# Performance work log

Hardware: AMD Instinct MI355X
Metric: run time of the kernel (lower is better)

Reference implementation:

```python
import jax, jax.numpy as jnp
import numpy as np

N_NODES = 100000
N_EDGES = 1600000
D_IN, D_HID, D_OUT = 128, 128, 64


def setup_inputs() -> dict:
    key = jax.random.key(0)
    ks = jax.random.split(key, 6)
    x = jax.random.normal(ks[0], (N_NODES, D_IN), dtype=jnp.float32)
    edge_index = jax.random.randint(ks[1], (2, N_EDGES), 0, N_NODES, dtype=jnp.int64)
    s1 = 1.0 / np.sqrt(D_IN)
    s2 = 1.0 / np.sqrt(D_HID)
    return {
        "x": x,
        "edge_index": edge_index,
        "Wl1": jax.random.uniform(ks[2], (D_HID, D_IN), jnp.float32, -s1, s1),
        "bl1": jnp.zeros((D_HID,), jnp.float32),
        "Wr1": jax.random.uniform(ks[3], (D_HID, D_IN), jnp.float32, -s1, s1),
        "Wl2": jax.random.uniform(ks[4], (D_OUT, D_HID), jnp.float32, -s2, s2),
        "bl2": jnp.zeros((D_OUT,), jnp.float32),
        "Wr2": jax.random.uniform(ks[5], (D_OUT, D_HID), jnp.float32, -s2, s2),
    }


def _sage_conv(x, src, dst, Wl, bl, Wr, n_nodes):
    # mean-aggregate neighbor features src -> dst
    agg = jax.ops.segment_sum(x[src], dst, num_segments=n_nodes)  # [N, d_in]
    deg = jax.ops.segment_sum(jnp.ones((src.shape[0],), x.dtype), dst, num_segments=n_nodes)
    agg = agg / jnp.maximum(deg, 1.0)[:, None]
    # PyG SAGEConv: lin_l(agg) + lin_r(x), bias only on lin_l
    return agg @ Wl.T + bl + x @ Wr.T


def reference(x, edge_index, Wl1, bl1, Wr1, Wl2, bl2, Wr2):
    src, dst = edge_index[0], edge_index[1]
    n = x.shape[0]
    h = _sage_conv(x, src, dst, Wl1, bl1, Wr1, n)
    h = jax.nn.relu(h)
    # dropout is identity in eval mode (training=False)
    out = _sage_conv(h, src, dst, Wl2, bl2, Wr2, n)
    return out
```

## Files before the change

kernel.cpp:

```cpp
#include <hip/hip_runtime.h>

#define N_NODES_C 100000
#define N_EDGES_C 1600000
#define NTILES_C 6250
#define CAP_C 48
#define NBUCK_C 196
#define BCAP_C 10240
#define EPB_C 4096

typedef __attribute__((ext_vector_type(8))) short short8;
typedef __attribute__((ext_vector_type(4))) short short4v;
typedef __attribute__((ext_vector_type(4))) float floatx4;

static __device__ __forceinline__ unsigned short f2bf(float f) {
    union { float f; unsigned int u; } c; c.f = f;
    unsigned int u = c.u;
    unsigned int lsb = (u >> 16) & 1u;
    u += 0x7fffu + lsb;
    return (unsigned short)(u >> 16);
}
static __device__ __forceinline__ float bf2f(unsigned short h) {
    union { unsigned int u; float f; } c; c.u = ((unsigned int)h) << 16;
    return c.f;
}

__global__ void bucket_kernel(const int* __restrict__ src, const int* __restrict__ dst,
                              int* __restrict__ gcur, int2* __restrict__ bucket, int E) {
    __shared__ int2 sedge[EPB_C];
    __shared__ int lcnt[NBUCK_C];
    __shared__ int lbase[NBUCK_C];
    __shared__ int lcur[NBUCK_C];
    const int tid = threadIdx.x;
    const int e0 = blockIdx.x * EPB_C;
    const int n = min(EPB_C, E - e0);

    if (tid < NBUCK_C) { lcnt[tid] = 0; lcur[tid] = 0; }
    for (int i = tid; i < n; i += 256) {
        sedge[i] = make_int2(src[e0 + i], dst[e0 + i]);
    }
    __syncthreads();
    for (int i = tid; i < n; i += 256) {
        atomicAdd(&lcnt[sedge[i].y >> 9], 1);
    }
    __syncthreads();
    if (tid < NBUCK_C) {
        int c = lcnt[tid];
        lbase[tid] = (c > 0) ? atomicAdd(&gcur[tid], c) : 0;
    }
    __syncthreads();
    for (int i = tid; i < n; i += 256) {
        int2 e = sedge[i];
        int b = e.y >> 9;
        int p = lbase[b] + atomicAdd(&lcur[b], 1);
        if (p < BCAP_C) bucket[b * BCAP_C + p] = e;
    }
}

__global__ void csr_build_kernel(const int* __restrict__ gcur, const int2* __restrict__ bucket,
                                 int* __restrict__ cnt, int* __restrict__ csr, int N) {
    __shared__ int lcnt[512];
    const int b = blockIdx.x;
    const int tid = threadIdx.x;
    const int d0 = b << 9;
    const int ne = min(gcur[b], BCAP_C);
    lcnt[tid] = 0; lcnt[tid + 256] = 0;
    __syncthreads();
    const int2* be = bucket + b * BCAP_C;
    for (int i = tid; i < ne; i += 256) {
        int2 e = be[i];
        int slot = atomicAdd(&lcnt[e.y - d0], 1);
        if (slot < CAP_C) csr[e.y * CAP_C + slot] = e.x;
    }
    __syncthreads();
    for (int d = tid; d < 512; d += 256) {
        int node = d0 + d;
        if (node < N) cnt[node] = lcnt[d];
    }
}

__global__ void pack1_kernel(const float* __restrict__ Wl, const float* __restrict__ Wr,
                             unsigned short* __restrict__ Bhi, unsigned short* __restrict__ Blo,
                             int total) {
    int t = blockIdx.x * 256 + threadIdx.x;
    if (t >= total) return;
    int j  = t & 7;
    int l  = (t >> 3) & 63;
    int ks = (t >> 9) & 7;
    int ct = t >> 12;
    int k = ks * 32 + ((l >> 4) << 3) + j;
    int o = ct * 16 + (l & 15);
    float v = (k < 128) ? Wl[o * 128 + k] : Wr[o * 128 + (k - 128)];
    unsigned short hi = f2bf(v);
    unsigned short lo = f2bf(v - bf2f(hi));
    Bhi[t] = hi;
    Blo[t] = lo;
}

__global__ void pack2_kernel(const float* __restrict__ Wl, const float* __restrict__ Wr,
                             unsigned short* __restrict__ Bhi, unsigned short* __restrict__ Blo,
                             int total) {
    int t = blockIdx.x * 256 + threadIdx.x;
    if (t >= total) return;
    int j  = t & 7;
    int l  = (t >> 3) & 63;
    int ks = (t >> 9) & 3;
    int ct = t >> 11;
    int k = ks * 32 + ((l >> 4) << 3) + j;
    int o = ct * 16 + (l & 15);
    float v = (o < 64) ? Wl[o * 128 + k] : Wr[(o - 64) * 128 + k];
    unsigned short hi = f2bf(v);
    unsigned short lo = f2bf(v - bf2f(hi));
    Bhi[t] = hi;
    Blo[t] = lo;
}

__global__ void tobf_kernel(const float* __restrict__ x, unsigned short* __restrict__ xb,
                            int total8) {
    int t = blockIdx.x * 256 + threadIdx.x;
    if (t >= total8) return;
    const float4* p = (const float4*)x;
    float4 a = p[(size_t)t * 2];
    float4 b = p[(size_t)t * 2 + 1];
    unsigned short r[8] = {f2bf(a.x), f2bf(a.y), f2bf(a.z), f2bf(a.w),
                           f2bf(b.x), f2bf(b.y), f2bf(b.z), f2bf(b.w)};
    *(uint4*)(xb + (size_t)t * 8) = *(uint4*)r;
}

static __device__ __forceinline__ void acc_add8(float* a, uint4 v) {
    unsigned int u[4] = {v.x, v.y, v.z, v.w};
#pragma unroll
    for (int i = 0; i < 4; i++) {
        union { unsigned int x; float f; } lo, hi;
        lo.x = u[i] << 16;
        hi.x = u[i] & 0xffff0000u;
        a[2 * i]     += lo.f;
        a[2 * i + 1] += hi.f;
    }
}

__global__ void agg_bf_kernel(const unsigned short* __restrict__ featb,
                              const int* __restrict__ cnt,
                              const int* __restrict__ csr,
                              unsigned short* __restrict__ aggb, int N) {
    int wid = (blockIdx.x * 256 + threadIdx.x) >> 6;
    if (wid >= N) return;
    int lane = threadIdx.x & 63;
    int q = lane >> 4;
    int c = lane & 15;
    int degc = cnt[wid];
    int deg = min(degc, CAP_C);
    const int* row = csr + wid * CAP_C;
    float acc0[8] = {0.f, 0.f, 0.f, 0.f, 0.f, 0.f, 0.f, 0.f};
    float acc1[8] = {0.f, 0.f, 0.f, 0.f, 0.f, 0.f, 0.f, 0.f};
    int e = q;
    for (; e + 4 < deg; e += 8) {
        int s0 = row[e];
        int s1 = row[e + 4];
        uint4 v0 = *(const uint4*)(featb + (size_t)s0 * 128 + c * 8);
        uint4 v1 = *(const uint4*)(featb + (size_t)s1 * 128 + c * 8);
        acc_add8(acc0, v0);
        acc_add8(acc1, v1);
    }
    if (e < deg) {
        int s0 = row[e];
        uint4 v0 = *(const uint4*)(featb + (size_t)s0 * 128 + c * 8);
        acc_add8(acc0, v0);
    }
    float acc[8];
#pragma unroll
    for (int j = 0; j < 8; j++) {
        float v = acc0[j] + acc1[j];
        v += __shfl_xor(v, 16, 64);
        v += __shfl_xor(v, 32, 64);
        acc[j] = v;
    }
    if (lane < 16) {
        float sc = 1.0f / fmaxf((float)degc, 1.0f);
        unsigned short r[8];
#pragma unroll
        for (int j = 0; j < 8; j++) r[j] = f2bf(acc[j] * sc);
        *(uint4*)(aggb + (size_t)wid * 128 + c * 8) = *(uint4*)r;
    }
}

__launch_bounds__(256, 2)
__global__ void gemm1_kernel(const unsigned short* __restrict__ aggb,
                             const float* __restrict__ xf,
                             const unsigned short* __restrict__ Bhi,
                             const unsigned short* __restrict__ Blo,
                             const float* __restrict__ bias,
                             unsigned short* __restrict__ hbf) {
    constexpr int CTW = 2, NACC = 2;
    __shared__ unsigned short sAhi[16][264];
    __shared__ unsigned short sAlo[16][136];

    const int wave = threadIdx.x >> 6;
    const int lane = threadIdx.x & 63;
    const int quad = lane >> 4;
    const int l16 = lane & 15;

    short8 bhi[CTW][8], blo[CTW][8];
    float bias_v[CTW];
#pragma unroll
    for (int i = 0; i < CTW; i++) {
        int ct = wave * CTW + i;
        bias_v[i] = bias[ct * 16 + l16];
#pragma unroll
        for (int ks = 0; ks < 8; ks++) {
            int off = ((ct * 8 + ks) * 64 + lane) * 8;
            bhi[i][ks] = *(const short8*)(Bhi + off);
            blo[i][ks] = *(const short8*)(Blo + off);
        }
    }

    const int tn = threadIdx.x >> 4;
    const int tc = threadIdx.x & 15;

    for (int tile = blockIdx.x; tile < NTILES_C; tile += gridDim.x) {
        const int node0 = tile * 16;
        const size_t rowa = (size_t)(node0 + tn) * 128;
        *(short8*)&sAhi[tn][tc * 8] = *(const short8*)(aggb + rowa + tc * 8);
#pragma unroll
        for (int r = 0; r < 2; r++) {
            int c2 = tc + r * 16;
            float4 v = *(const float4*)(xf + rowa + c2 * 4);
            short4v hi, lo;
            unsigned short h0 = f2bf(v.x); hi.x = (short)h0; lo.x = (short)f2bf(v.x - bf2f(h0));
            unsigned short h1 = f2bf(v.y); hi.y = (short)h1; lo.y = (short)f2bf(v.y - bf2f(h1));
            unsigned short h2 = f2bf(v.z); hi.z = (short)h2; lo.z = (short)f2bf(v.z - bf2f(h2));
            unsigned short h3 = f2bf(v.w); hi.w = (short)h3; lo.w = (short)f2bf(v.w - bf2f(h3));
            *(short4v*)&sAhi[tn][128 + c2 * 4] = hi;
            *(short4v*)&sAlo[tn][c2 * 4]       = lo;
        }
        __syncthreads();

        floatx4 acc[CTW][NACC];
#pragma unroll
        for (int i = 0; i < CTW; i++)
#pragma unroll
            for (int p = 0; p < NACC; p++)
                acc[i][p] = (floatx4){0.f, 0.f, 0.f, 0.f};

#pragma unroll
        for (int ks = 0; ks < 8; ks++) {
            short8 ahi = *(const short8*)&sAhi[l16][ks * 32 + quad * 8];
            int p = ks & 1;
            if (ks < 4) {
#pragma unroll
                for (int i = 0; i < CTW; i++) {
                    acc[i][p] = __builtin_amdgcn_mfma_f32_16x16x32_bf16(ahi, bhi[i][ks], acc[i][p], 0, 0, 0);
                    acc[i][p] = __builtin_amdgcn_mfma_f32_16x16x32_bf16(ahi, blo[i][ks], acc[i][p], 0, 0, 0);
                }
            } else {
                short8 alo = *(const short8*)&sAlo[l16][(ks - 4) * 32 + quad * 8];
#pragma unroll
                for (int i = 0; i < CTW; i++) {
                    acc[i][p] = __builtin_amdgcn_mfma_f32_16x16x32_bf16(ahi, bhi[i][ks], acc[i][p], 0, 0, 0);
                    acc[i][p] = __builtin_amdgcn_mfma_f32_16x16x32_bf16(alo, bhi[i][ks], acc[i][p], 0, 0, 0);
                    acc[i][p] = __builtin_amdgcn_mfma_f32_16x16x32_bf16(ahi, blo[i][ks], acc[i][p], 0, 0, 0);
                }
            }
        }

#pragma unroll
        for (int i = 0; i < CTW; i++) {
            floatx4 s = acc[i][0];
            s.x += acc[i][1].x; s.y += acc[i][1].y;
            s.z += acc[i][1].z; s.w += acc[i][1].w;
            int o = (wave * CTW + i) * 16 + l16;
            float vals[4] = {s.x, s.y, s.z, s.w};
#pragma unroll
            for (int r = 0; r < 4; r++) {
                int node = node0 + quad * 4 + r;
                float v = fmaxf(vals[r] + bias_v[i], 0.f);
                hbf[(size_t)node * 128 + o] = f2bf(v);
            }
        }
        __syncthreads();
    }
}

__launch_bounds__(256, 2)
__global__ void gemm2_kernel(const unsigned short* __restrict__ hbf,
                             const unsigned short* __restrict__ Bhi,
                             const unsigned short* __restrict__ Blo,
                             const float* __restrict__ bias,
                             unsigned short* __restrict__ g,
                             unsigned short* __restrict__ s2b) {
    constexpr int CTW = 2, NACC = 2;
    __shared__ unsigned short sA[16][136];

    const int wave = threadIdx.x >> 6;
    const int lane = threadIdx.x & 63;
    const int quad = lane >> 4;
    const int l16 = lane & 15;

    short8 bhi[CTW][4], blo[CTW][4];
    float bias_v[CTW];
#pragma unroll
    for (int i = 0; i < CTW; i++) {
        int ct = wave * CTW + i;
        int o = ct * 16 + l16;
        bias_v[i] = (o >= 64) ? bias[o - 64] : 0.f;
#pragma unroll
        for (int ks = 0; ks < 4; ks++) {
            int off = ((ct * 4 + ks) * 64 + lane) * 8;
            bhi[i][ks] = *(const short8*)(Bhi + off);
            blo[i][ks] = *(const short8*)(Blo + off);
        }
    }

    const int tn = threadIdx.x >> 4;
    const int tc = threadIdx.x & 15;

    for (int tile = blockIdx.x; tile < NTILES_C; tile += gridDim.x) {
        const int node0 = tile * 16;
        *(short8*)&sA[tn][tc * 8] = *(const short8*)(hbf + (size_t)(node0 + tn) * 128 + tc * 8);
        __syncthreads();

        floatx4 acc[CTW][NACC];
#pragma unroll
        for (int i = 0; i < CTW; i++)
#pragma unroll
            for (int p = 0; p < NACC; p++)
                acc[i][p] = (floatx4){0.f, 0.f, 0.f, 0.f};

#pragma unroll
        for (int ks = 0; ks < 4; ks++) {
            short8 ahi = *(const short8*)&sA[l16][ks * 32 + quad * 8];
            int p = ks & 1;
#pragma unroll
            for (int i = 0; i < CTW; i++) {
                acc[i][p] = __builtin_amdgcn_mfma_f32_16x16x32_bf16(ahi, bhi[i][ks], acc[i][p], 0, 0, 0);
                acc[i][p] = __builtin_amdgcn_mfma_f32_16x16x32_bf16(ahi, blo[i][ks], acc[i][p], 0, 0, 0);
            }
        }

#pragma unroll
        for (int i = 0; i < CTW; i++) {
            floatx4 s = acc[i][0];
            s.x += acc[i][1].x; s.y += acc[i][1].y;
            s.z += acc[i][1].z; s.w += acc[i][1].w;
            int o = (wave * CTW + i) * 16 + l16;
            float vals[4] = {s.x, s.y, s.z, s.w};
#pragma unroll
            for (int r = 0; r < 4; r++) {
                int node = node0 + quad * 4 + r;
                float v = vals[r] + bias_v[i];
                if (o < 64) g[(size_t)node * 64 + o] = f2bf(v);
                else        s2b[(size_t)node * 64 + (o - 64)] = f2bf(v);
            }
        }
        __syncthreads();
    }
}

static __device__ __forceinline__ void acc_add4(float* a, uint2 v) {
    unsigned int u[2] = {v.x, v.y};
#pragma unroll
    for (int i = 0; i < 2; i++) {
        union { unsigned int x; float f; } lo, hi;
        lo.x = u[i] << 16;
        hi.x = u[i] & 0xffff0000u;
        a[2 * i]     += lo.f;
        a[2 * i + 1] += hi.f;
    }
}

__global__ void agg2e_kernel(const unsigned short* __restrict__ g,
                             const unsigned short* __restrict__ s2b,
                             const int* __restrict__ cnt,
                             const int* __restrict__ csr,
                             float* __restrict__ out, int N) {
    int wid = (blockIdx.x * 256 + threadIdx.x) >> 6;
    if (wid >= N) return;
    int lane = threadIdx.x & 63;
    int q = lane >> 4;
    int c = lane & 15;
    int degc = cnt[wid];
    int deg = min(degc, CAP_C);
    const int* row = csr + wid * CAP_C;
    float acc0[4] = {0.f, 0.f, 0.f, 0.f};
    float acc1[4] = {0.f, 0.f, 0.f, 0.f};
    int e = q;
    for (; e + 4 < deg; e += 8) {
        int s0 = row[e];
        int s1 = row[e + 4];
        uint2 v0 = *(const uint2*)(g + (size_t)s0 * 64 + c * 4);
        uint2 v1 = *(const uint2*)(g + (size_t)s1 * 64 + c * 4);
        acc_add4(acc0, v0);
        acc_add4(acc1, v1);
    }
    if (e < deg) {
        int s0 = row[e];
        uint2 v0 = *(const uint2*)(g + (size_t)s0 * 64 + c * 4);
        acc_add4(acc0, v0);
    }
    float acc[4];
#pragma unroll
    for (int j = 0; j < 4; j++) {
        float v = acc0[j] + acc1[j];
        v += __shfl_xor(v, 16, 64);
        v += __shfl_xor(v, 32, 64);
        acc[j] = v;
    }
    if (lane < 16) {
        float sc = 1.0f / fmaxf((float)degc, 1.0f);
        uint2 sv = *(const uint2*)(s2b + (size_t)wid * 64 + c * 4);
        float s[4];
        {
            union { unsigned int x; float f; } t0, t1, t2, t3;
            t0.x = sv.x << 16; t1.x = sv.x & 0xffff0000u;
            t2.x = sv.y << 16; t3.x = sv.y & 0xffff0000u;
            s[0] = t0.f; s[1] = t1.f; s[2] = t2.f; s[3] = t3.f;
        }
        float4 r;
        r.x = acc[0] * sc + s[0];
        r.y = acc[1] * sc + s[1];
        r.z = acc[2] * sc + s[2];
        r.w = acc[3] * sc + s[3];
        *(float4*)(out + (size_t)wid * 64 + c * 4) = r;
    }
}

extern "C" void kernel_launch(void* const* d_in, const int* in_sizes, int n_in,
                              void* d_out, int out_size, void* d_ws, size_t ws_size,
                              hipStream_t stream) {
    const float* x    = (const float*)d_in[0];
    const int*   ei   = (const int*)d_in[1];
    const float* Wl1  = (const float*)d_in[2];
    const float* bl1  = (const float*)d_in[3];
    const float* Wr1  = (const float*)d_in[4];
    const float* Wl2  = (const float*)d_in[5];
    const float* bl2  = (const float*)d_in[6];
    const float* Wr2  = (const float*)d_in[7];
    float* out = (float*)d_out;

    const int N = N_NODES_C;
    const int E = N_EDGES_C;
    const int* src = ei;
    const int* dst = ei + E;

    char* ws = (char*)d_ws;
    unsigned short* B1hi = (unsigned short*)(ws + 0);
    unsigned short* B1lo = (unsigned short*)(ws + 65536);
    unsigned short* B2hi = (unsigned short*)(ws + 131072);
    unsigned short* B2lo = (unsigned short*)(ws + 163840);
    int*   cnt  = (int*)  (ws + 196608);
    int*   gcur = (int*)  (ws + 598016);
    int*   csr  = (int*)  (ws + 1048576);
    unsigned short* xbf  = (unsigned short*)(ws + 20248576);
    unsigned short* aggb = (unsigned short*)(ws + 45848576);
    unsigned short* hbf  = (unsigned short*)(ws + 71448576);
    unsigned short* g    = aggb;
    unsigned short* s2b  = aggb + 6400000;
    int2*  bucket = (int2*)hbf;

    hipMemsetAsync(gcur, 0, NBUCK_C * sizeof(int), stream);
    bucket_kernel<<<(E + EPB_C - 1) / EPB_C, 256, 0, stream>>>(src, dst, gcur, bucket, E);
    csr_build_kernel<<<NBUCK_C, 256, 0, stream>>>(gcur, bucket, cnt, csr, N);

    pack1_kernel<<<128, 256, 0, stream>>>(Wl1, Wr1, B1hi, B1lo, 128 * 256);
    pack2_kernel<<<64, 256, 0, stream>>>(Wl2, Wr2, B2hi, B2lo, 128 * 128);
    tobf_kernel<<<(N * 16 + 255) / 256, 256, 0, stream>>>(x, xbf, N * 16);

    agg_bf_kernel<<<(N + 3) / 4, 256, 0, stream>>>(xbf, cnt, csr, aggb, N);
    gemm1_kernel<<<512, 256, 0, stream>>>(aggb, x, B1hi, B1lo, bl1, hbf);

    gemm2_kernel<<<512, 256, 0, stream>>>(hbf, B2hi, B2lo, bl2, g, s2b);
    agg2e_kernel<<<(N + 3) / 4, 256, 0, stream>>>(g, s2b, cnt, csr, out, N);
}
```

Measured before the change: 293.5 us.

## Build compact CSR with prefix offsets, fuse prep kernels, widen GEMM tiles

Replaces the fixed-capacity padded neighbor lists (48 slots per node) with a compact CSR. Buckets now hold 256 nodes each, and every edge is packed into a single int. A per-bucket prefix scan produces node offsets, which are stored in a nodeinfo array. The two weight-packing kernels and the fp32-to-bf16 conversion of x are merged into one launch. The aggregation loops are unrolled to four independent accumulators, and both GEMM kernels process 32-node tiles instead of 16. The aim is to cut CSR memory traffic, the cost of the padded layout, and launch overhead, and to expose more memory-level parallelism. The trade-offs are a serial prefix sum over bucket counts done by thread 0 in every block, and more shared memory in csr_build.

```diff
diff --git a/kernel.cpp b/kernel.cpp
--- a/kernel.cpp
+++ b/kernel.cpp
@@ -2,10 +2,9 @@
 
 #define N_NODES_C 100000
 #define N_EDGES_C 1600000
-#define NTILES_C 6250
-#define CAP_C 48
-#define NBUCK_C 196
-#define BCAP_C 10240
+#define NT32_C 3125
+#define NBUCK_C 392
+#define BCAP_C 4800
 #define EPB_C 4096
 
 typedef __attribute__((ext_vector_type(8))) short short8;
@@ -25,8 +24,9 @@
 }
 
 __global__ void bucket_kernel(const int* __restrict__ src, const int* __restrict__ dst,
-                              int* __restrict__ gcur, int2* __restrict__ bucket, int E) {
-    __shared__ int2 sedge[EPB_C];
+                              int* __restrict__ gcur, int* __restrict__ bucket, int E) {
+    __shared__ int ssrc[EPB_C];
+    __shared__ int sdst[EPB_C];
     __shared__ int lcnt[NBUCK_C];
     __shared__ int lbase[NBUCK_C];
     __shared__ int lcur[NBUCK_C];
@@ -34,96 +34,123 @@
     const int e0 = blockIdx.x * EPB_C;
     const int n = min(EPB_C, E - e0);
 
-    if (tid < NBUCK_C) { lcnt[tid] = 0; lcur[tid] = 0; }
+    for (int i = tid; i < NBUCK_C; i += 256) { lcnt[i] = 0; lcur[i] = 0; }
     for (int i = tid; i < n; i += 256) {
-        sedge[i] = make_int2(src[e0 + i], dst[e0 + i]);
+        ssrc[i] = src[e0 + i];
+        sdst[i] = dst[e0 + i];
     }
     __syncthreads();
     for (int i = tid; i < n; i += 256) {
-        atomicAdd(&lcnt[sedge[i].y >> 9], 1);
-    }
-    __syncthreads();
-    if (tid < NBUCK_C) {
-        int c = lcnt[tid];
-        lbase[tid] = (c > 0) ? atomicAdd(&gcur[tid], c) : 0;
+        atomicAdd(&lcnt[sdst[i] >> 8], 1);
+    }
+    __syncthreads();
+    for (int i = tid; i < NBUCK_C; i += 256) {
+        int c = lcnt[i];
+        lbase[i] = (c > 0) ? atomicAdd(&gcur[i], c) : 0;
     }
     __syncthreads();
     for (int i = tid; i < n; i += 256) {
-        int2 e = sedge[i];
-        int b = e.y >> 9;
+        int d = sdst[i];
+        int b = d >> 8;
         int p = lbase[b] + atomicAdd(&lcur[b], 1);
-        if (p < BCAP_C) bucket[b * BCAP_C + p] = e;
-    }
-}
-
-__global__ void csr_build_kernel(const int* __restrict__ gcur, const int2* __restrict__ bucket,
-                                 int* __restrict__ cnt, int* __restrict__ csr, int N) {
-    __shared__ int lcnt[512];
+        if (p < BCAP_C) bucket[b * BCAP_C + p] = (ssrc[i] << 8) | (d & 255);
+    }
+}
+
+__global__ void csr_build_kernel(const int* __restrict__ gcur, const int* __restrict__ bucket,
+                                 int2* __restrict__ nodeinfo, int* __restrict__ csr, int N) {
+    __shared__ int sg[NBUCK_C];
+    __shared__ int lcnt[256];
+    __shared__ int lcur[256];
+    __shared__ int sc[2][256];
+    __shared__ int eord[BCAP_C];
+    __shared__ int sbase_s;
     const int b = blockIdx.x;
     const int tid = threadIdx.x;
-    const int d0 = b << 9;
     const int ne = min(gcur[b], BCAP_C);
-    lcnt[tid] = 0; lcnt[tid + 256] = 0;
-    __syncthreads();
-    const int2* be = bucket + b * BCAP_C;
+
+    for (int i = tid; i < NBUCK_C; i += 256) sg[i] = min(gcur[i], BCAP_C);
+    lcnt[tid] = 0;
+    lcur[tid] = 0;
+    __syncthreads();
+    if (tid == 0) {
+        int s = 0;
+        for (int i = 0; i < b; i++) s += sg[i];
+        sbase_s = s;
+    }
+    const int* be = bucket + b * BCAP_C;
     for (int i = tid; i < ne; i += 256) {
-        int2 e = be[i];
-        int slot = atomicAdd(&lcnt[e.y - d0], 1);
-        if (slot < CAP_C) csr[e.y * CAP_C + slot] = e.x;
-    }
-    __syncthreads();
-    for (int d = tid; d < 512; d += 256) {
-        int node = d0 + d;
-        if (node < N) cnt[node] = lcnt[d];
-    }
-}
-
-__global__ void pack1_kernel(const float* __restrict__ Wl, const float* __restrict__ Wr,
-                             unsigned short* __restrict__ Bhi, unsigned short* __restrict__ Blo,
-                             int total) {
-    int t = blockIdx.x * 256 + threadIdx.x;
-    if (t >= total) return;
-    int j  = t & 7;
-    int l  = (t >> 3) & 63;
-    int ks = (t >> 9) & 7;
-    int ct = t >> 12;
-    int k = ks * 32 + ((l >> 4) << 3) + j;
-    int o = ct * 16 + (l & 15);
-    float v = (k < 128) ? Wl[o * 128 + k] : Wr[o * 128 + (k - 128)];
-    unsigned short hi = f2bf(v);
-    unsigned short lo = f2bf(v - bf2f(hi));
-    Bhi[t] = hi;
-    Blo[t] = lo;
-}
-
-__global__ void pack2_kernel(const float* __restrict__ Wl, const float* __restrict__ Wr,
-                             unsigned short* __restrict__ Bhi, unsigned short* __restrict__ Blo,
-                             int total) {
-    int t = blockIdx.x * 256 + threadIdx.x;
-    if (t >= total) return;
-    int j  = t & 7;
-    int l  = (t >> 3) & 63;
-    int ks = (t >> 9) & 3;
-    int ct = t >> 11;
-    int k = ks * 32 + ((l >> 4) << 3) + j;
-    int o = ct * 16 + (l & 15);
-    float v = (o < 64) ? Wl[o * 128 + k] : Wr[(o - 64) * 128 + k];
-    unsigned short hi = f2bf(v);
-    unsigned short lo = f2bf(v - bf2f(hi));
-    Bhi[t] = hi;
-    Blo[t] = lo;
-}
-
-__global__ void tobf_kernel(const float* __restrict__ x, unsigned short* __restrict__ xb,
-                            int total8) {
-    int t = blockIdx.x * 256 + threadIdx.x;
-    if (t >= total8) return;
-    const float4* p = (const float4*)x;
-    float4 a = p[(size_t)t * 2];
-    float4 b = p[(size_t)t * 2 + 1];
-    unsigned short r[8] = {f2bf(a.x), f2bf(a.y), f2bf(a.z), f2bf(a.w),
-                           f2bf(b.x), f2bf(b.y), f2bf(b.z), f2bf(b.w)};
-    *(uint4*)(xb + (size_t)t * 8) = *(uint4*)r;
+        atomicAdd(&lcnt[be[i] & 255], 1);
+    }
+    __syncthreads();
+    sc[0][tid] = lcnt[tid];
+    __syncthreads();
+    int cur = 0;
+    for (int off = 1; off < 256; off <<= 1) {
+        int v = sc[cur][tid] + ((tid >= off) ? sc[cur][tid - off] : 0);
+        sc[1 - cur][tid] = v;
+        __syncthreads();
+        cur ^= 1;
+    }
+    for (int i = tid; i < ne; i += 256) {
+        int p = be[i];
+        int dl = p & 255;
+        int slot = atomicAdd(&lcur[dl], 1);
+        int pre = (dl == 0) ? 0 : sc[cur][dl - 1];
+        eord[pre + slot] = p >> 8;
+    }
+    __syncthreads();
+    const int sbase = sbase_s;
+    for (int i = tid; i < ne; i += 256) csr[sbase + i] = eord[i];
+    int node = (b << 8) + tid;
+    if (node < N) {
+        int pre = (tid == 0) ? 0 : sc[cur][tid - 1];
+        nodeinfo[node] = make_int2(sbase + pre, lcnt[tid]);
+    }
+}
+
+__global__ void prep_kernel(const float* __restrict__ Wl1, const float* __restrict__ Wr1,
+                            const float* __restrict__ Wl2, const float* __restrict__ Wr2,
+                            const float* __restrict__ x,
+                            unsigned short* __restrict__ B1hi, unsigned short* __restrict__ B1lo,
+                            unsigned short* __restrict__ B2hi, unsigned short* __restrict__ B2lo,
+                            unsigned short* __restrict__ xb) {
+    int blk = blockIdx.x;
+    int tid = threadIdx.x;
+    if (blk < 128) {
+        int t = blk * 256 + tid;
+        int j  = t & 7;
+        int l  = (t >> 3) & 63;
+        int ks = (t >> 9) & 7;
+        int ct = t >> 12;
+        int k = ks * 32 + ((l >> 4) << 3) + j;
+        int o = ct * 16 + (l & 15);
+        float v = (k < 128) ? Wl1[o * 128 + k] : Wr1[o * 128 + (k - 128)];
+        unsigned short hi = f2bf(v);
+        B1hi[t] = hi;
+        B1lo[t] = f2bf(v - bf2f(hi));
+    } else if (blk < 192) {
+        int t = (blk - 128) * 256 + tid;
+        int j  = t & 7;
+        int l  = (t >> 3) & 63;
+        int ks = (t >> 9) & 3;
+        int ct = t >> 11;
+        int k = ks * 32 + ((l >> 4) << 3) + j;
+        int o = ct * 16 + (l & 15);
+        float v = (o < 64) ? Wl2[o * 128 + k] : Wr2[(o - 64) * 128 + k];
+        unsigned short hi = f2bf(v);
+        B2hi[t] = hi;
+        B2lo[t] = f2bf(v - bf2f(hi));
+    } else {
+        int t = (blk - 192) * 256 + tid;
+        if (t >= N_NODES_C * 16) return;
+        const float4* p = (const float4*)x;
+        float4 a = p[(size_t)t * 2];
+        float4 bb = p[(size_t)t * 2 + 1];
+        unsigned short r[8] = {f2bf(a.x), f2bf(a.y), f2bf(a.z), f2bf(a.w),
+                               f2bf(bb.x), f2bf(bb.y), f2bf(bb.z), f2bf(bb.w)};
+        *(uint4*)(xb + (size_t)t * 8) = *(uint4*)r;
+    }
 }
 
 static __device__ __forceinline__ void acc_add8(float* a, uint4 v) {
@@ -139,7 +166,7 @@
 }
 
 __global__ void agg_bf_kernel(const unsigned short* __restrict__ featb,
-                              const int* __restrict__ cnt,
+                              const int2* __restrict__ nodeinfo,
                               const int* __restrict__ csr,
                               unsigned short* __restrict__ aggb, int N) {
     int wid = (blockIdx.x * 256 + threadIdx.x) >> 6;
@@ -147,35 +174,43 @@
     int lane = threadIdx.x & 63;
     int q = lane >> 4;
     int c = lane & 15;
-    int degc = cnt[wid];
-    int deg = min(degc, CAP_C);
-    const int* row = csr + wid * CAP_C;
-    float acc0[8] = {0.f, 0.f, 0.f, 0.f, 0.f, 0.f, 0.f, 0.f};
-    float acc1[8] = {0.f, 0.f, 0.f, 0.f, 0.f, 0.f, 0.f, 0.f};
+    int2 info = nodeinfo[wid];
+    const int* row = csr + info.x;
+    const int deg = info.y;
+    float a0[8] = {0,0,0,0,0,0,0,0};
+    float a1[8] = {0,0,0,0,0,0,0,0};
+    float a2[8] = {0,0,0,0,0,0,0,0};
+    float a3[8] = {0,0,0,0,0,0,0,0};
     int e = q;
-    for (; e + 4 < deg; e += 8) {
+    for (; e + 12 < deg; e += 16) {
         int s0 = row[e];
         int s1 = row[e + 4];
+        int s2 = row[e + 8];
+        int s3 = row[e + 12];
         uint4 v0 = *(const uint4*)(featb + (size_t)s0 * 128 + c * 8);
         uint4 v1 = *(const uint4*)(featb + (size_t)s1 * 128 + c * 8);
-        acc_add8(acc0, v0);
-        acc_add8(acc1, v1);
-    }
-    if (e < deg) {
+        uint4 v2 = *(const uint4*)(featb + (size_t)s2 * 128 + c * 8);
+        uint4 v3 = *(const uint4*)(featb + (size_t)s3 * 128 + c * 8);
+        acc_add8(a0, v0);
+        acc_add8(a1, v1);
+        acc_add8(a2, v2);
+        acc_add8(a3, v3);
+    }
+    for (; e < deg; e += 4) {
         int s0 = row[e];
         uint4 v0 = *(const uint4*)(featb + (size_t)s0 * 128 + c * 8);
-        acc_add8(acc0, v0);
+        acc_add8(a0, v0);
     }
     float acc[8];
 #pragma unroll
     for (int j = 0; j < 8; j++) {
-        float v = acc0[j] + acc1[j];
+        float v = (a0[j] + a1[j]) + (a2[j] + a3[j]);
         v += __shfl_xor(v, 16, 64);
         v += __shfl_xor(v, 32, 64);
         acc[j] = v;
     }
     if (lane < 16) {
-        float sc = 1.0f / fmaxf((float)degc, 1.0f);
+        float sc = 1.0f / fmaxf((float)deg, 1.0f);
         unsigned short r[8];
 #pragma unroll
         for (int j = 0; j < 8; j++) r[j] = f2bf(acc[j] * sc);
@@ -190,20 +225,19 @@
                              const unsigned short* __restrict__ Blo,
                              const float* __restrict__ bias,
                              unsigned short* __restrict__ hbf) {
-    constexpr int CTW = 2, NACC = 2;
-    __shared__ unsigned short sAhi[16][264];
-    __shared__ unsigned short sAlo[16][136];
+    __shared__ unsigned short sAhi[32][264];
+    __shared__ unsigned short sAlo[32][136];
 
     const int wave = threadIdx.x >> 6;
     const int lane = threadIdx.x & 63;
     const int quad = lane >> 4;
     const int l16 = lane & 15;
 
-    short8 bhi[CTW][8], blo[CTW][8];
-    float bias_v[CTW];
-#pragma unroll
-    for (int i = 0; i < CTW; i++) {
-        int ct = wave * CTW + i;
+    short8 bhi[2][8], blo[2][8];
+    float bias_v[2];
+#pragma unroll
+    for (int i = 0; i < 2; i++) {
+        int ct = wave * 2 + i;
         bias_v[i] = bias[ct * 16 + l16];
 #pragma unroll
         for (int ks = 0; ks < 8; ks++) {
@@ -213,67 +247,74 @@
         }
     }
 
-    const int tn = threadIdx.x >> 4;
-    const int tc = threadIdx.x & 15;
-
-    for (int tile = blockIdx.x; tile < NTILES_C; tile += gridDim.x) {
-        const int node0 = tile * 16;
-        const size_t rowa = (size_t)(node0 + tn) * 128;
-        *(short8*)&sAhi[tn][tc * 8] = *(const short8*)(aggb + rowa + tc * 8);
-#pragma unroll
-        for (int r = 0; r < 2; r++) {
-            int c2 = tc + r * 16;
-            float4 v = *(const float4*)(xf + rowa + c2 * 4);
+    const int tid = threadIdx.x;
+
+    for (int tile = blockIdx.x; tile < NT32_C; tile += gridDim.x) {
+        const int node0 = tile * 32;
+        for (int u = tid; u < 512; u += 256) {
+            int n = u >> 4, cc = u & 15;
+            *(short8*)&sAhi[n][cc * 8] =
+                *(const short8*)(aggb + (size_t)(node0 + n) * 128 + cc * 8);
+        }
+        for (int u = tid; u < 1024; u += 256) {
+            int n = u >> 5, c2 = u & 31;
+            float4 v = *(const float4*)(xf + (size_t)(node0 + n) * 128 + c2 * 4);
             short4v hi, lo;
             unsigned short h0 = f2bf(v.x); hi.x = (short)h0; lo.x = (short)f2bf(v.x - bf2f(h0));
             unsigned short h1 = f2bf(v.y); hi.y = (short)h1; lo.y = (short)f2bf(v.y - bf2f(h1));
             unsigned short h2 = f2bf(v.z); hi.z = (short)h2; lo.z = (short)f2bf(v.z - bf2f(h2));
             unsigned short h3 = f2bf(v.w); hi.w = (short)h3; lo.w = (short)f2bf(v.w - bf2f(h3));
-            *(short4v*)&sAhi[tn][128 + c2 * 4] = hi;
-            *(short4v*)&sAlo[tn][c2 * 4]       = lo;
+            *(short4v*)&sAhi[n][128 + c2 * 4] = hi;
+            *(short4v*)&sAlo[n][c2 * 4]       = lo;
         }
         __syncthreads();
 
-        floatx4 acc[CTW][NACC];
-#pragma unroll
-        for (int i = 0; i < CTW; i++)
-#pragma unroll
-            for (int p = 0; p < NACC; p++)
-                acc[i][p] = (floatx4){0.f, 0.f, 0.f, 0.f};
+        floatx4 acc[2][2];
+#pragma unroll
+        for (int i = 0; i < 2; i++)
+#pragma unroll
+            for (int s = 0; s < 2; s++)
+                acc[i][s] = (floatx4){0.f, 0.f, 0.f, 0.f};
 
 #pragma unroll
         for (int ks = 0; ks < 8; ks++) {
-            short8 ahi = *(const short8*)&sAhi[l16][ks * 32 + quad * 8];
-            int p = ks & 1;
+            short8 a0 = *(const short8*)&sAhi[l16][ks * 32 + quad * 8];
+            short8 a1 = *(const short8*)&sAhi[16 + l16][ks * 32 + quad * 8];
             if (ks < 4) {
 #pragma unroll
-                for (int i = 0; i < CTW; i++) {
-                    acc[i][p] = __builtin_amdgcn_mfma_f32_16x16x32_bf16(ahi, bhi[i][ks], acc[i][p], 0, 0, 0);
-                    acc[i][p] = __builtin_amdgcn_mfma_f32_16x16x32_bf16(ahi, blo[i][ks], acc[i][p], 0, 0, 0);
+                for (int i = 0; i < 2; i++) {
+                    acc[i][0] = __builtin_amdgcn_mfma_f32_16x16x32_bf16(a0, bhi[i][ks], acc[i][0], 0, 0, 0);
+                    acc[i][0] = __builtin_amdgcn_mfma_f32_16x16x32_bf16(a0, blo[i][ks], acc[i][0], 0, 0, 0);
+                    acc[i][1] = __builtin_amdgcn_mfma_f32_16x16x32_bf16(a1, bhi[i][ks], acc[i][1], 0, 0, 0);
+                    acc[i][1] = __builtin_amdgcn_mfma_f32_16x16x32_bf16(a1, blo[i][ks], acc[i][1], 0, 0, 0);
                 }
             } else {
-                short8 alo = *(const short8*)&sAlo[l16][(ks - 4) * 32 + quad * 8];
-#pragma unroll
-                for (int i = 0; i < CTW; i++) {
-                    acc[i][p] = __builtin_amdgcn_mfma_f32_16x16x32_bf16(ahi, bhi[i][ks], acc[i][p], 0, 0, 0);
-                    acc[i][p] = __builtin_amdgcn_mfma_f32_16x16x32_bf16(alo, bhi[i][ks], acc[i][p], 0, 0, 0);
-                    acc[i][p] = __builtin_amdgcn_mfma_f32_16x16x32_bf16(ahi, blo[i][ks], acc[i][p], 0, 0, 0);
+                short8 a0l = *(const short8*)&sAlo[l16][(ks - 4) * 32 + quad * 8];
+                short8 a1l = *(const short8*)&sAlo[16 + l16][(ks - 4) * 32 + quad * 8];
+#pragma unroll
+                for (int i = 0; i < 2; i++) {
+                    acc[i][0] = __builtin_amdgcn_mfma_f32_16x16x32_bf16(a0, bhi[i][ks], acc[i][0], 0, 0, 0);
+                    acc[i][0] = __builtin_amdgcn_mfma_f32_16x16x32_bf16(a0l, bhi[i][ks], acc[i][0], 0, 0, 0);
+                    acc[i][0] = __builtin_amdgcn_mfma_f32_16x16x32_bf16(a0, blo[i][ks], acc[i][0], 0, 0, 0);
+                    acc[i][1] = __builtin_amdgcn_mfma_f32_16x16x32_bf16(a1, bhi[i][ks], acc[i][1], 0, 0, 0);
+                    acc[i][1] = __builtin_amdgcn_mfma_f32_16x16x32_bf16(a1l, bhi[i][ks], acc[i][1], 0, 0, 0);
+                    acc[i][1] = __builtin_amdgcn_mfma_f32_16x16x32_bf16(a1, blo[i][ks], acc[i][1], 0, 0, 0);
                 }
             }
         }
 
 #pragma unroll
-        for (int i = 0; i < CTW; i++) {
-            floatx4 s = acc[i][0];
-            s.x += acc[i][1].x; s.y += acc[i][1].y;
-            s.z += acc[i][1].z; s.w += acc[i][1].w;
-            int o = (wave * CTW + i) * 16 + l16;
-            float vals[4] = {s.x, s.y, s.z, s.w};
-#pragma unroll
-            for (int r = 0; r < 4; r++) {
-                int node = node0 + quad * 4 + r;
-                float v = fmaxf(vals[r] + bias_v[i], 0.f);
-                hbf[(size_t)node * 128 + o] = f2bf(v);
+        for (int i = 0; i < 2; i++) {
+            int o = wave * 32 + i * 16 + l16;
+#pragma unroll
+            for (int s = 0; s < 2; s++) {
+                float vals[4] = {acc[i][s].x, acc[i][s].y, acc[i][s].z, acc[i][s].w};
+#pragma unroll
+                for (int r = 0; r < 4; r++) {
+                    int node = node0 + s * 16 + quad * 4 + r;
+                    float v = fmaxf(vals[r] + bias_v[i], 0.f);
+                    hbf[(size_t)node * 128 + o] = f2bf(v);
+                }
             }
         }
         __syncthreads();
@@ -287,19 +328,18 @@
                              const float* __restrict__ bias,
                              unsigned short* __restrict__ g,
                              unsigned short* __restrict__ s2b) {
-    constexpr int CTW = 2, NACC = 2;
-    __shared__ unsigned short sA[16][136];
+    __shared__ unsigned short sA[32][136];
 
     const int wave = threadIdx.x >> 6;
     const int lane = threadIdx.x & 63;
     const int quad = lane >> 4;
     const int l16 = lane & 15;
 
-    short8 bhi[CTW][4], blo[CTW][4];
-    float bias_v[CTW];
-#pragma unroll
-    for (int i = 0; i < CTW; i++) {
-        int ct = wave * CTW + i;
+    short8 bhi[2][4], blo[2][4];
+    float bias_v[2];
+#pragma unroll
+    for (int i = 0; i < 2; i++) {
+        int ct = wave * 2 + i;
         int o = ct * 16 + l16;
         bias_v[i] = (o >= 64) ? bias[o - 64] : 0.f;
 #pragma unroll
@@ -310,45 +350,50 @@
         }
     }
 
-    const int tn = threadIdx.x >> 4;
-    const int tc = threadIdx.x & 15;
-
-    for (int tile = blockIdx.x; tile < NTILES_C; tile += gridDim.x) {
-        const int node0 = tile * 16;
-        *(short8*)&sA[tn][tc * 8] = *(const short8*)(hbf + (size_t)(node0 + tn) * 128 + tc * 8);
+    const int tid = threadIdx.x;
+
+    for (int tile = blockIdx.x; tile < NT32_C; tile += gridDim.x) {
+        const int node0 = tile * 32;
+        for (int u = tid; u < 512; u += 256) {
+            int n = u >> 4, cc = u & 15;
+            *(short8*)&sA[n][cc * 8] =
+                *(const short8*)(hbf + (size_t)(node0 + n) * 128 + cc * 8);
+        }
         __syncthreads();
 
-        floatx4 acc[CTW][NACC];
-#pragma unroll
-        for (int i = 0; i < CTW; i++)
-#pragma unroll
-            for (int p = 0; p < NACC; p++)
-                acc[i][p] = (floatx4){0.f, 0.f, 0.f, 0.f};
+        floatx4 acc[2][2];
+#pragma unroll
+        for (int i = 0; i < 2; i++)
+#pragma unroll
+            for (int s = 0; s < 2; s++)
+                acc[i][s] = (floatx4){0.f, 0.f, 0.f, 0.f};
 
 #pragma unroll
         for (int ks = 0; ks < 4; ks++) {
-            short8 ahi = *(const short8*)&sA[l16][ks * 32 + quad * 8];
-            int p = ks & 1;
-#pragma unroll
-            for (int i = 0; i < CTW; i++) {
-                acc[i][p] = __builtin_amdgcn_mfma_f32_16x16x32_bf16(ahi, bhi[i][ks], acc[i][p], 0, 0, 0);
-                acc[i][p] = __builtin_amdgcn_mfma_f32_16x16x32_bf16(ahi, blo[i][ks], acc[i][p], 0, 0, 0);
+            short8 a0 = *(const short8*)&sA[l16][ks * 32 + quad * 8];
+            short8 a1 = *(const short8*)&sA[16 + l16][ks * 32 + quad * 8];
+#pragma unroll
+            for (int i = 0; i < 2; i++) {
+                acc[i][0] = __builtin_amdgcn_mfma_f32_16x16x32_bf16(a0, bhi[i][ks], acc[i][0], 0, 0, 0);
+                acc[i][0] = __builtin_amdgcn_mfma_f32_16x16x32_bf16(a0, blo[i][ks], acc[i][0], 0, 0, 0);
+                acc[i][1] = __builtin_amdgcn_mfma_f32_16x16x32_bf16(a1, bhi[i][ks], acc[i][1], 0, 0, 0);
+                acc[i][1] = __builtin_amdgcn_mfma_f32_16x16x32_bf16(a1, blo[i][ks], acc[i][1], 0, 0, 0);
             }
         }
 
 #pragma unroll
-        for (int i = 0; i < CTW; i++) {
-            floatx4 s = acc[i][0];
-            s.x += acc[i][1].x; s.y += acc[i][1].y;
-            s.z += acc[i][1].z; s.w += acc[i][1].w;
-            int o = (wave * CTW + i) * 16 + l16;
-            float vals[4] = {s.x, s.y, s.z, s.w};
-#pragma unroll
-            for (int r = 0; r < 4; r++) {
-                int node = node0 + quad * 4 + r;
-                float v = vals[r] + bias_v[i];
-                if (o < 64) g[(size_t)node * 64 + o] = f2bf(v);
-                else        s2b[(size_t)node * 64 + (o - 64)] = f2bf(v);
+        for (int i = 0; i < 2; i++) {
+            int o = wave * 32 + i * 16 + l16;
+#pragma unroll
+            for (int s = 0; s < 2; s++) {
+                float vals[4] = {acc[i][s].x, acc[i][s].y, acc[i][s].z, acc[i][s].w};
+#pragma unroll
+                for (int r = 0; r < 4; r++) {
+                    int node = node0 + s * 16 + quad * 4 + r;
+                    float v = vals[r] + bias_v[i];
+                    if (o < 64) g[(size_t)node * 64 + o] = f2bf(v);
+                    else        s2b[(size_t)node * 64 + (o - 64)] = f2bf(v);
+                }
             }
         }
         __syncthreads();
@@ -369,7 +414,7 @@
 
 __global__ void agg2e_kernel(const unsigned short* __restrict__ g,
                              const unsigned short* __restrict__ s2b,
-                             const int* __restrict__ cnt,
+                             const int2* __restrict__ nodeinfo,
                              const int* __restrict__ csr,
                              float* __restrict__ out, int N) {
     int wid = (blockIdx.x * 256 + threadIdx.x) >> 6;
@@ -377,35 +422,43 @@
     int lane = threadIdx.x & 63;
     int q = lane >> 4;
     int c = lane & 15;
-    int degc = cnt[wid];
-    int deg = min(degc, CAP_C);
-    const int* row = csr + wid * CAP_C;
-    float acc0[4] = {0.f, 0.f, 0.f, 0.f};
-    float acc1[4] = {0.f, 0.f, 0.f, 0.f};
+    int2 info = nodeinfo[wid];
+    const int* row = csr + info.x;
+    const int deg = info.y;
+    float a0[4] = {0,0,0,0};
+    float a1[4] = {0,0,0,0};
+    float a2[4] = {0,0,0,0};
+    float a3[4] = {0,0,0,0};
     int e = q;
-    for (; e + 4 < deg; e += 8) {
+    for (; e + 12 < deg; e += 16) {
         int s0 = row[e];
         int s1 = row[e + 4];
+        int s2 = row[e + 8];
+        int s3 = row[e + 12];
         uint2 v0 = *(const uint2*)(g + (size_t)s0 * 64 + c * 4);
         uint2 v1 = *(const uint2*)(g + (size_t)s1 * 64 + c * 4);
-        acc_add4(acc0, v0);
-        acc_add4(acc1, v1);
-    }
-    if (e < deg) {
+        uint2 v2 = *(const uint2*)(g + (size_t)s2 * 64 + c * 4);
+        uint2 v3 = *(const uint2*)(g + (size_t)s3 * 64 + c * 4);
+        acc_add4(a0, v0);
+        acc_add4(a1, v1);
+        acc_add4(a2, v2);
+        acc_add4(a3, v3);
+    }
+    for (; e < deg; e += 4) {
         int s0 = row[e];
         uint2 v0 = *(const uint2*)(g + (size_t)s0 * 64 + c * 4);
-        acc_add4(acc0, v0);
+        acc_add4(a0, v0);
     }
     float acc[4];
 #pragma unroll
     for (int j = 0; j < 4; j++) {
-        float v = acc0[j] + acc1[j];
+        float v = (a0[j] + a1[j]) + (a2[j] + a3[j]);
         v += __shfl_xor(v, 16, 64);
         v += __shfl_xor(v, 32, 64);
         acc[j] = v;
     }
     if (lane < 16) {
-        float sc = 1.0f / fmaxf((float)degc, 1.0f);
+        float sc = 1.0f / fmaxf((float)deg, 1.0f);
         uint2 sv = *(const uint2*)(s2b + (size_t)wid * 64 + c * 4);
         float s[4];
         {
@@ -446,27 +499,26 @@
     unsigned short* B1lo = (unsigned short*)(ws + 65536);
     unsigned short* B2hi = (unsigned short*)(ws + 131072);
     unsigned short* B2lo = (unsigned short*)(ws + 163840);
-    int*   cnt  = (int*)  (ws + 196608);
-    int*   gcur = (int*)  (ws + 598016);
+    int2*  nodeinfo = (int2*)(ws + 196608);
+    int*   gcur = (int*)  (ws + 998400);
     int*   csr  = (int*)  (ws + 1048576);
     unsigned short* xbf  = (unsigned short*)(ws + 20248576);
     unsigned short* aggb = (unsigned short*)(ws + 45848576);
     unsigned short* hbf  = (unsigned short*)(ws + 71448576);
     unsigned short* g    = aggb;
     unsigned short* s2b  = aggb + 6400000;
-    int2*  bucket = (int2*)hbf;
+    int*   bucket = (int*)hbf;
 
     hipMemsetAsync(gcur, 0, NBUCK_C * sizeof(int), stream);
     bucket_kernel<<<(E + EPB_C - 1) / EPB_C, 256, 0, stream>>>(src, dst, gcur, bucket, E);
-    csr_build_kernel<<<NBUCK_C, 256, 0, stream>>>(gcur, bucket, cnt, csr, N);
-
-    pack1_kernel<<<128, 256, 0, stream>>>(Wl1, Wr1, B1hi, B1lo, 128 * 256);
-    pack2_kernel<<<64, 256, 0, stream>>>(Wl2, Wr2, B2hi, B2lo, 128 * 128);
-    tobf_kernel<<<(N * 16 + 255) / 256, 256, 0, stream>>>(x, xbf, N * 16);
-
-    agg_bf_kernel<<<(N + 3) / 4, 256, 0, stream>>>(xbf, cnt, csr, aggb, N);
+    csr_build_kernel<<<NBUCK_C, 256, 0, stream>>>(gcur, bucket, nodeinfo, csr, N);
+
+    prep_kernel<<<192 + (N * 16 + 255) / 256, 256, 0, stream>>>(
+        Wl1, Wr1, Wl2, Wr2, x, B1hi, B1lo, B2hi, B2lo, xbf);
+
+    agg_bf_kernel<<<(N + 3) / 4, 256, 0, stream>>>(xbf, nodeinfo, csr, aggb, N);
     gemm1_kernel<<<512, 256, 0, stream>>>(aggb, x, B1hi, B1lo, bl1, hbf);
 
     gemm2_kernel<<<512, 256, 0, stream>>>(hbf, B2hi, B2lo, bl2, g, s2b);
-    agg2e_kernel<<<(N + 3) / 4, 256, 0, stream>>>(g, s2b, cnt, csr, out, N);
-}
+    agg2e_kernel<<<(N + 3) / 4, 256, 0, stream>>>(g, s2b, nodeinfo, csr, out, N);
+}
```

After: 299.6 us. +2.1%, slower.
